# Kernel optimization log

Hardware: AMD Instinct MI355X
Metric: run time of the kernel (lower is better)

## Reference

```python
import jax, jax.numpy as jnp
import numpy as np
from jax import lax

B, T, I, H, O = 512, 4096, 1, 16, 1  # batch, seq_len, input_size, hidden_size, output_size


def setup_inputs() -> dict:
    key = jax.random.key(0)
    ks = jax.random.split(key, 7)
    s = 1.0 / np.sqrt(H)  # PyTorch uniform(-1/sqrt(H), 1/sqrt(H)) init scale
    u = lambda k, shape: jax.random.uniform(k, shape, jnp.float32, -s, s)
    return {
        "x": jax.random.normal(ks[0], (B, T, I), jnp.float32),
        "W_ih": u(ks[1], (4 * H, I)),
        "W_hh": u(ks[2], (4 * H, H)),
        "b_ih": u(ks[3], (4 * H,)),
        "b_hh": u(ks[4], (4 * H,)),
        "W_fc": u(ks[5], (O, H)),
        "b_fc": u(ks[6], (O,)),
    }


def reference(x, W_ih, W_hh, b_ih, b_hh, W_fc, b_fc):
    # Single-layer LSTM, batch_first, dropout forced to 0 when n_layers==1.
    # Precompute input projection for all timesteps (hoisted out of the scan).
    xW = jnp.einsum('bti,gi->btg', x, W_ih) + b_ih + b_hh  # [B, T, 4H]
    xW_t = jnp.swapaxes(xW, 0, 1)  # [T, B, 4H]

    def step(carry, xt):
        h, c = carry
        gates = xt + h @ W_hh.T  # [B, 4H]; PyTorch gate order: i, f, g, o
        i, f, g, o = jnp.split(gates, 4, axis=-1)
        i = jax.nn.sigmoid(i)
        f = jax.nn.sigmoid(f)
        g = jnp.tanh(g)
        o = jax.nn.sigmoid(o)
        c = f * c + i * g
        h = o * jnp.tanh(c)
        return (h, c), h

    h0 = jnp.zeros((B, H), x.dtype)
    c0 = jnp.zeros((B, H), x.dtype)
    _, hs = lax.scan(step, (h0, c0), xW_t)  # hs: [T, B, H]
    hs = jnp.swapaxes(hs, 0, 1)  # [B, T, H]
    out = hs @ W_fc.T + b_fc  # [B, T, O]
    return out
```

## Files before the change

kernel.cpp:

```cpp
#include <hip/hip_runtime.h>
#include <hip/hip_bf16.h>


constexpr int NB = 512;
constexpr int NT = 4096;

template<int CTRL>
__device__ __forceinline__ float qbcast(float x) {
  return __int_as_float(__builtin_amdgcn_mov_dpp(__float_as_int(x), CTRL, 0xF, 0xF, true));
}
__device__ __forceinline__ float rdlane(float x, int lane) {
  return __int_as_float(__builtin_amdgcn_readlane(__float_as_int(x), lane));
}
__device__ __forceinline__ float vexp2(float x) {
  float r; asm("v_exp_f32 %0, %1" : "=v"(r) : "v"(x)); return r;
}
__device__ __forceinline__ float vrcp(float x) {
  float r; asm("v_rcp_f32 %0, %1" : "=v"(r) : "v"(x)); return r;
}

__global__ __launch_bounds__(64, 1) void lstm_fused(
    const float* __restrict__ x,
    const float* __restrict__ W_ih,
    const float* __restrict__ W_hh,
    const float* __restrict__ b_ih,
    const float* __restrict__ b_hh,
    const float* __restrict__ W_fc,
    const float* __restrict__ b_fc,
    float* __restrict__ out)
{
  __shared__ float tile[64 * 65];
  const int b = blockIdx.x;
  const int l = threadIdx.x;
  const int j = l >> 2;
  const int k = l & 3;
  const int r = k * 16 + j;

  constexpr float LOG2E = 1.4426950408889634f;
  constexpr float K2    = -2.0f * LOG2E;
  const float sc = (k == 2) ? K2 : -LOG2E;

  float wrow[16];
  #pragma unroll
  for (int q = 0; q < 16; ++q) wrow[q] = W_hh[r * 16 + q] * sc;
  const float wx    = W_ih[r] * sc;
  const float wb    = (b_ih[r] + b_hh[r]) * sc;
  const float act_m = (k == 2) ? (2.0f * K2) : 1.0f;
  const float act_a = (k == 2) ? (-K2)       : 0.0f;
  const float wfc   = W_fc[j] * 0.25f;
  const float bfc   = b_fc[0];

  const float* xb = x + (size_t)b * NT;
  float*       ob = out + (size_t)b * NT;

  float cs = 0.0f;
  float sh[16];
  #pragma unroll
  for (int q = 0; q < 16; ++q) sh[q] = 0.0f;

  float xcur = xb[l];

  for (int blk = 0; blk < NT / 64; ++blk) {
    float xnext = 0.0f;
    if (blk + 1 < NT / 64) xnext = xb[(blk + 1) * 64 + l];

    #pragma unroll 16
    for (int tt = 0; tt < 64; ++tt) {
      const float sx    = rdlane(xcur, tt);
      const float xinit = fmaf(wx, sx, wb);
      float a0 = fmaf(wrow[0], sh[0], xinit);
      float a1 = wrow[1] * sh[1];
      float a2 = wrow[2] * sh[2];
      float a3 = wrow[3] * sh[3];
      #pragma unroll
      for (int q = 4; q < 16; q += 4) {
        a0 = fmaf(wrow[q + 0], sh[q + 0], a0);
        a1 = fmaf(wrow[q + 1], sh[q + 1], a1);
        a2 = fmaf(wrow[q + 2], sh[q + 2], a2);
        a3 = fmaf(wrow[q + 3], sh[q + 3], a3);
      }
      const float z   = (a0 + a1) + (a2 + a3);
      const float e1  = vexp2(z);
      const float r1  = vrcp(1.0f + e1);
      const float act = fmaf(r1, act_m, act_a);
      const float ii  = qbcast<0x00>(act);
      const float ff  = qbcast<0x55>(act);
      const float ggs = qbcast<0xAA>(act);
      const float oo  = qbcast<0xFF>(act);
      const float oo2 = oo + oo;
      cs = fmaf(ff, cs, ii * ggs);
      const float e2 = vexp2(cs);
      const float r2 = vrcp(1.0f + e2);
      const float h  = fmaf(oo2, r2, -oo);
      tile[tt * 65 + l] = h * wfc;
      #pragma unroll
      for (int q = 0; q < 16; ++q) sh[q] = rdlane(h, 4 * q);
    }

    float s0 = bfc, s1 = 0.0f, s2 = 0.0f, s3 = 0.0f;
    #pragma unroll
    for (int i2 = 0; i2 < 64; i2 += 4) {
      s0 += tile[l * 65 + i2 + 0];
      s1 += tile[l * 65 + i2 + 1];
      s2 += tile[l * 65 + i2 + 2];
      s3 += tile[l * 65 + i2 + 3];
    }
    ob[blk * 64 + l] = (s0 + s1) + (s2 + s3);
    xcur = xnext;
  }
}

extern "C" void kernel_launch(void* const* d_in, const int* in_sizes, int n_in,
                              void* d_out, int out_size, void* d_ws, size_t ws_size,
                              hipStream_t stream) {
  const float* x    = (const float*)d_in[0];
  const float* W_ih = (const float*)d_in[1];
  const float* W_hh = (const float*)d_in[2];
  const float* b_ih = (const float*)d_in[3];
  const float* b_hh = (const float*)d_in[4];
  const float* W_fc = (const float*)d_in[5];
  const float* b_fc = (const float*)d_in[6];
  float* out = (float*)d_out;
  (void)in_sizes; (void)n_in; (void)out_size; (void)d_ws; (void)ws_size;
  lstm_fused<<<NB, 64, 0, stream>>>(x, W_ih, W_hh, b_ih, b_hh, W_fc, b_fc, out);
}
```

Measured before the change: 464.1 us.

## Interleave two independent batch sequences per wavefront to hide recurrence latency

```diff
diff --git a/kernel.cpp b/kernel.cpp
--- a/kernel.cpp
+++ b/kernel.cpp
@@ -29,8 +29,10 @@
     const float* __restrict__ b_fc,
     float* __restrict__ out)
 {
-  __shared__ float tile[64 * 65];
-  const int b = blockIdx.x;
+  __shared__ float tile0[64 * 65];
+  __shared__ float tile1[64 * 65];
+  const int b0 = blockIdx.x * 2;
+  const int b1 = b0 + 1;
   const int l = threadIdx.x;
   const int j = l >> 2;
   const int k = l & 3;
@@ -50,63 +52,109 @@
   const float wfc   = W_fc[j] * 0.25f;
   const float bfc   = b_fc[0];
 
-  const float* xb = x + (size_t)b * NT;
-  float*       ob = out + (size_t)b * NT;
+  const float* xb0 = x + (size_t)b0 * NT;
+  const float* xb1 = x + (size_t)b1 * NT;
+  float*       ob0 = out + (size_t)b0 * NT;
+  float*       ob1 = out + (size_t)b1 * NT;
 
-  float cs = 0.0f;
-  float sh[16];
+  float cs0 = 0.0f, cs1 = 0.0f;
+  float sh0[16], sh1[16];
   #pragma unroll
-  for (int q = 0; q < 16; ++q) sh[q] = 0.0f;
+  for (int q = 0; q < 16; ++q) { sh0[q] = 0.0f; sh1[q] = 0.0f; }
 
-  float xcur = xb[l];
+  float xcur0 = xb0[l];
+  float xcur1 = xb1[l];
 
   for (int blk = 0; blk < NT / 64; ++blk) {
-    float xnext = 0.0f;
-    if (blk + 1 < NT / 64) xnext = xb[(blk + 1) * 64 + l];
+    float xnext0 = 0.0f, xnext1 = 0.0f;
+    if (blk + 1 < NT / 64) {
+      xnext0 = xb0[(blk + 1) * 64 + l];
+      xnext1 = xb1[(blk + 1) * 64 + l];
+    }
 
-    #pragma unroll 16
+    #pragma unroll 8
     for (int tt = 0; tt < 64; ++tt) {
-      const float sx    = rdlane(xcur, tt);
-      const float xinit = fmaf(wx, sx, wb);
-      float a0 = fmaf(wrow[0], sh[0], xinit);
-      float a1 = wrow[1] * sh[1];
-      float a2 = wrow[2] * sh[2];
-      float a3 = wrow[3] * sh[3];
+      const float sx0    = rdlane(xcur0, tt);
+      const float sx1    = rdlane(xcur1, tt);
+      const float xinit0 = fmaf(wx, sx0, wb);
+      const float xinit1 = fmaf(wx, sx1, wb);
+
+      float a00 = fmaf(wrow[0], sh0[0], xinit0);
+      float a10 = fmaf(wrow[0], sh1[0], xinit1);
+      float a01 = wrow[1] * sh0[1];
+      float a11 = wrow[1] * sh1[1];
+      float a02 = wrow[2] * sh0[2];
+      float a12 = wrow[2] * sh1[2];
+      float a03 = wrow[3] * sh0[3];
+      float a13 = wrow[3] * sh1[3];
       #pragma unroll
       for (int q = 4; q < 16; q += 4) {
-        a0 = fmaf(wrow[q + 0], sh[q + 0], a0);
-        a1 = fmaf(wrow[q + 1], sh[q + 1], a1);
-        a2 = fmaf(wrow[q + 2], sh[q + 2], a2);
-        a3 = fmaf(wrow[q + 3], sh[q + 3], a3);
+        a00 = fmaf(wrow[q + 0], sh0[q + 0], a00);
+        a10 = fmaf(wrow[q + 0], sh1[q + 0], a10);
+        a01 = fmaf(wrow[q + 1], sh0[q + 1], a01);
+        a11 = fmaf(wrow[q + 1], sh1[q + 1], a11);
+        a02 = fmaf(wrow[q + 2], sh0[q + 2], a02);
+        a12 = fmaf(wrow[q + 2], sh1[q + 2], a12);
+        a03 = fmaf(wrow[q + 3], sh0[q + 3], a03);
+        a13 = fmaf(wrow[q + 3], sh1[q + 3], a13);
       }
-      const float z   = (a0 + a1) + (a2 + a3);
-      const float e1  = vexp2(z);
-      const float r1  = vrcp(1.0f + e1);
-      const float act = fmaf(r1, act_m, act_a);
-      const float ii  = qbcast<0x00>(act);
-      const float ff  = qbcast<0x55>(act);
-      const float ggs = qbcast<0xAA>(act);
-      const float oo  = qbcast<0xFF>(act);
-      const float oo2 = oo + oo;
-      cs = fmaf(ff, cs, ii * ggs);
-      const float e2 = vexp2(cs);
-      const float r2 = vrcp(1.0f + e2);
-      const float h  = fmaf(oo2, r2, -oo);
-      tile[tt * 65 + l] = h * wfc;
+      const float z0 = (a00 + a01) + (a02 + a03);
+      const float z1 = (a10 + a11) + (a12 + a13);
+
+      const float e10 = vexp2(z0);
+      const float e11 = vexp2(z1);
+      const float r10 = vrcp(1.0f + e10);
+      const float r11 = vrcp(1.0f + e11);
+      const float act0 = fmaf(r10, act_m, act_a);
+      const float act1 = fmaf(r11, act_m, act_a);
+
+      const float ii0  = qbcast<0x00>(act0);
+      const float ii1  = qbcast<0x00>(act1);
+      const float ff0  = qbcast<0x55>(act0);
+      const float ff1  = qbcast<0x55>(act1);
+      const float ggs0 = qbcast<0xAA>(act0);
+      const float ggs1 = qbcast<0xAA>(act1);
+      const float oo0  = qbcast<0xFF>(act0);
+      const float oo1  = qbcast<0xFF>(act1);
+      const float oo20 = oo0 + oo0;
+      const float oo21 = oo1 + oo1;
+
+      cs0 = fmaf(ff0, cs0, ii0 * ggs0);
+      cs1 = fmaf(ff1, cs1, ii1 * ggs1);
+      const float e20 = vexp2(cs0);
+      const float e21 = vexp2(cs1);
+      const float r20 = vrcp(1.0f + e20);
+      const float r21 = vrcp(1.0f + e21);
+      const float h0  = fmaf(oo20, r20, -oo0);
+      const float h1  = fmaf(oo21, r21, -oo1);
+
+      tile0[tt * 65 + l] = h0 * wfc;
+      tile1[tt * 65 + l] = h1 * wfc;
+
       #pragma unroll
-      for (int q = 0; q < 16; ++q) sh[q] = rdlane(h, 4 * q);
+      for (int q = 0; q < 16; ++q) {
+        sh0[q] = rdlane(h0, 4 * q);
+        sh1[q] = rdlane(h1, 4 * q);
+      }
     }
 
-    float s0 = bfc, s1 = 0.0f, s2 = 0.0f, s3 = 0.0f;
+    float s00 = bfc, s01 = 0.0f, s02 = 0.0f, s03 = 0.0f;
+    float s10 = bfc, s11 = 0.0f, s12 = 0.0f, s13 = 0.0f;
     #pragma unroll
     for (int i2 = 0; i2 < 64; i2 += 4) {
-      s0 += tile[l * 65 + i2 + 0];
-      s1 += tile[l * 65 + i2 + 1];
-      s2 += tile[l * 65 + i2 + 2];
-      s3 += tile[l * 65 + i2 + 3];
+      s00 += tile0[l * 65 + i2 + 0];
+      s10 += tile1[l * 65 + i2 + 0];
+      s01 += tile0[l * 65 + i2 + 1];
+      s11 += tile1[l * 65 + i2 + 1];
+      s02 += tile0[l * 65 + i2 + 2];
+      s12 += tile1[l * 65 + i2 + 2];
+      s03 += tile0[l * 65 + i2 + 3];
+      s13 += tile1[l * 65 + i2 + 3];
     }
-    ob[blk * 64 + l] = (s0 + s1) + (s2 + s3);
-    xcur = xnext;
+    ob0[blk * 64 + l] = (s00 + s01) + (s02 + s03);
+    ob1[blk * 64 + l] = (s10 + s11) + (s12 + s13);
+    xcur0 = xnext0;
+    xcur1 = xnext1;
   }
 }
 
@@ -122,5 +170,5 @@
   const float* b_fc = (const float*)d_in[6];
   float* out = (float*)d_out;
   (void)in_sizes; (void)n_in; (void)out_size; (void)d_ws; (void)ws_size;
-  lstm_fused<<<NB, 64, 0, stream>>>(x, W_ih, W_hh, b_ih, b_hh, W_fc, b_fc, out);
+  lstm_fused<<<NB / 2, 64, 0, stream>>>(x, W_ih, W_hh, b_ih, b_hh, W_fc, b_fc, out);
 }
```

After: 820.3 us. +76.8%, slower.
